# Kernel tuning notes

Hardware: AMD Instinct MI355X
Metric: run time of the kernel (lower is better)

The kernel has to match this reference:

```python
import jax, jax.numpy as jnp
import numpy as np

N, C, R = 8192, 512, 8
DK = C // R  # 64

def setup_inputs() -> dict:
    key = jax.random.key(0)
    k1, k2, kq, kk, kv = jax.random.split(key, 5)
    s = 0.05
    return {
        "im1": jax.random.normal(k1, (N, C), jnp.float32),
        "im2": jax.random.normal(k2, (N, C), jnp.float32),
        "Wq": jax.random.normal(kq, (C, DK), jnp.float32) * s,
        "Wk": jax.random.normal(kk, (C, DK), jnp.float32) * s,
        "Wv": jax.random.normal(kv, (C, C), jnp.float32) * s,
    }

def reference(im1, im2, Wq, Wk, Wv):
    # shared projections (weights stored as [in, out]; torch Linear is x @ W.T)
    im1_q = im1 @ Wq  # [N, DK]
    im1_k = im1 @ Wk  # [N, DK]
    im1_v = im1 @ Wv  # [N, C]
    im2_q = im2 @ Wq
    im2_k = im2 @ Wk
    im2_v = im2 @ Wv
    # cross attention (no scaling in original)
    im1_attn = jax.nn.softmax(im2_q @ im1_k.T, axis=-1)  # [N, N]
    im2_attn = jax.nn.softmax(im1_q @ im2_k.T, axis=-1)  # [N, N]
    im1_out = im1_attn @ im1_v + im1
    im2_out = im2_attn @ im2_v + im2
    return im1_out, im2_out
```

## Files before the change

### kernel.cpp

```cpp
#include <hip/hip_runtime.h>

#define NN 8192
#define CC 512
#define DKK 64

typedef float f32x4 __attribute__((ext_vector_type(4)));
typedef float f32x16 __attribute__((ext_vector_type(16)));
typedef _Float16 f16x8 __attribute__((ext_vector_type(8)));
typedef _Float16 f16x4 __attribute__((ext_vector_type(4)));

__device__ __forceinline__ f32x4 mfma16(f16x8 a, f16x8 b, f32x4 c) {
    return __builtin_amdgcn_mfma_f32_16x16x32_f16(a, b, c, 0, 0, 0);
}
__device__ __forceinline__ f32x16 mfma32(f16x8 a, f16x8 b, f32x16 c) {
    return __builtin_amdgcn_mfma_f32_32x32x16_f16(a, b, c, 0, 0, 0);
}
__device__ __forceinline__ f16x8 scl8(f16x8 v, float f) {
    _Float16 h = (_Float16)f;
    f16x8 r;
#pragma unroll
    for (int i = 0; i < 8; i++) r[i] = v[i] * h;
    return r;
}

__global__ void wtrans_all_kernel(const float* __restrict__ Wq, const float* __restrict__ Wk,
                                  const float* __restrict__ Wv,
                                  _Float16* __restrict__ Wqt, _Float16* __restrict__ Wkt,
                                  _Float16* __restrict__ Wvf) {
    int idx = blockIdx.x * 256 + threadIdx.x;
    if (idx < 32768) {
        int n = idx >> 9, k = idx & 511;
        Wqt[idx] = (_Float16)Wq[k * 64 + n];
    } else if (idx < 65536) {
        int j = idx - 32768;
        int n = j >> 9, k = j & 511;
        Wkt[j] = (_Float16)Wk[k * 64 + n];
    } else {
        int j = idx - 65536;
        int k16 = j & 15, c = (j >> 4) & 511, ks = j >> 13;
        Wvf[j] = (_Float16)Wv[(size_t)(16 * ks + k16) * 512 + c];
    }
}

__global__ __launch_bounds__(256) void proj_qk2_kernel(
    const float* __restrict__ im1, const float* __restrict__ im2,
    const _Float16* __restrict__ Wqt, const _Float16* __restrict__ Wkt,
    _Float16* __restrict__ Q1, _Float16* __restrict__ Kf1,
    _Float16* __restrict__ Q2, _Float16* __restrict__ Kf2)
{
    const float* X = blockIdx.y ? im2 : im1;
    _Float16* Q = blockIdx.y ? Q2 : Q1;
    _Float16* Kf = blockIdx.y ? Kf2 : Kf1;

    __shared__ __align__(16) _Float16 Wlds[128 * 512];

    const int tid = threadIdx.x;
    const int lane = tid & 63, wave = tid >> 6;
    const int n16 = lane & 15, quad = lane >> 4;

#pragma unroll
    for (int i = 0; i < 32; i++) {
        const int idx = tid + 256 * i;
        const int row = idx >> 6, ch = idx & 63;
        const _Float16* src = (row < 64) ? (Wqt + (size_t)row * 512 + ch * 8)
                                         : (Wkt + (size_t)(row - 64) * 512 + ch * 8);
        *(f16x8*)&Wlds[row * 512 + ((ch ^ (row & 7)) * 8)] = *(const f16x8*)src;
    }
    __syncthreads();

    const int arow = blockIdx.x * 64 + wave * 16 + n16;
    f32x4 acc[8];
#pragma unroll
    for (int i = 0; i < 8; i++) acc[i] = (f32x4){0.f, 0.f, 0.f, 0.f};

    const float* xbase = X + (size_t)arow * 512 + quad * 8;
    for (int kk = 0; kk < 16; kk++) {
        f32x4 xa = *(const f32x4*)(xbase + kk * 32);
        f32x4 xb = *(const f32x4*)(xbase + kk * 32 + 4);
        f16x8 afrag;
#pragma unroll
        for (int j = 0; j < 4; j++) { afrag[j] = (_Float16)xa[j]; afrag[4 + j] = (_Float16)xb[j]; }
#pragma unroll
        for (int t = 0; t < 8; t++) {
            const int row = t * 16 + n16;
            f16x8 bfr = *(const f16x8*)&Wlds[row * 512 + (((4 * kk + quad) ^ (row & 7)) * 8)];
            acc[t] = mfma16(afrag, bfr, acc[t]);
        }
    }
    const int rbase = blockIdx.x * 64 + wave * 16 + quad * 4;
#pragma unroll
    for (int t = 0; t < 4; t++)
#pragma unroll
        for (int r = 0; r < 4; r++) {
            Q[(size_t)(rbase + r) * 64 + t * 16 + n16] = (_Float16)acc[t][r];
            Kf[((size_t)(blockIdx.x * 4 + t) * 64 + (wave * 16 + quad * 4 + r)) * 16 + n16] =
                (_Float16)acc[4 + t][r];
        }
}

__global__ __launch_bounds__(256) void proj_vt_kernel(
    const float* __restrict__ im1, const float* __restrict__ im2,
    const _Float16* __restrict__ Wvf,
    _Float16* __restrict__ Vf1, _Float16* __restrict__ Vf2)
{
    const float* X = blockIdx.y ? im2 : im1;
    _Float16* Vf = blockIdx.y ? Vf2 : Vf1;
    const int n0 = blockIdx.x * 32;
    const int tid = threadIdx.x;
    const int lane = tid & 63, wave = tid >> 6;
    const int l31 = lane & 31, lhi = lane >> 5;

    __shared__ __align__(16) _Float16 Xlds[32 * 512];

#pragma unroll
    for (int i = 0; i < 8; i++) {
        const int n = tid >> 3;
        const int chunk = (tid & 7) + 8 * i;
        const float* xp = X + (size_t)(n0 + n) * CC + chunk * 8;
        f32x4 x0 = *(const f32x4*)xp;
        f32x4 x1 = *(const f32x4*)(xp + 4);
        f16x8 d;
#pragma unroll
        for (int j = 0; j < 4; j++) { d[j] = (_Float16)x0[j]; d[4 + j] = (_Float16)x1[j]; }
        *(f16x8*)&Xlds[n * 512 + ((chunk ^ (n & 7)) * 8)] = d;
    }
    __syncthreads();

    f32x16 acc[4];
#pragma unroll
    for (int t = 0; t < 4; t++)
#pragma unroll
        for (int r = 0; r < 16; r++) acc[t][r] = 0.f;

    for (int ks = 0; ks < 32; ks++) {
        f16x8 xb = *(const f16x8*)&Xlds[l31 * 512 + (((2 * ks + lhi) ^ (l31 & 7)) * 8)];
#pragma unroll
        for (int ct = 0; ct < 4; ct++) {
            const _Float16* wp = Wvf + ((size_t)ks * 512 + 128 * wave + 32 * ct + l31) * 16 + 8 * lhi;
            acc[ct] = mfma32(*(const f16x8*)wp, xb, acc[ct]);
        }
    }
    const int tile = n0 >> 6;
    const int ksbase = (n0 & 32) >> 4;
#pragma unroll
    for (int ct = 0; ct < 4; ct++)
#pragma unroll
        for (int r = 0; r < 16; r++) {
            const int c = 128 * wave + 32 * ct + (r & 3) + 8 * (r >> 2) + 4 * lhi;
            const int ks = ksbase + (l31 >> 4);
            Vf[((size_t)(tile * 4 + ks) * 512 + c) * 16 + (l31 & 15)] = (_Float16)acc[ct][r];
        }
}

__global__ __launch_bounds__(1024, 4) void flash7_kernel(
    const _Float16* __restrict__ Q1, const _Float16* __restrict__ Kf1,
    const _Float16* __restrict__ Q2, const _Float16* __restrict__ Kf2,
    const _Float16* __restrict__ Vf1, const _Float16* __restrict__ Vf2,
    const float* __restrict__ im1, const float* __restrict__ im2,
    float* __restrict__ out)
{
    const int bid = blockIdx.x;
    const int img = bid & 1;
    const int qbase = (bid >> 1) * 64;
    const _Float16* Q = img ? Q1 : Q2;
    const _Float16* Kf = img ? Kf2 : Kf1;
    const _Float16* Vf = img ? Vf2 : Vf1;
    const float* res = img ? im2 : im1;
    float* o = out + (size_t)img * NN * CC;

    __shared__ __align__(16) _Float16 P[2][4][8][64][8];
    __shared__ float mPart[2][4][2][64];
    __shared__ float mF[4][2][64], lF[4][2][64];

    const int tid = threadIdx.x;
    const int lane = tid & 63, w = tid >> 6;
    const int l31 = lane & 31, lhi = lane >> 5;
    const int g = w >> 2, a = (w >> 1) & 1, b = w & 1;

    f16x8 qf[4];
    {
        const _Float16* qp = Q + (size_t)(qbase + 32 * b + l31) * DKK + 8 * lhi;
#pragma unroll
        for (int k = 0; k < 4; k++) qf[k] = *(const f16x8*)(qp + 16 * k);
    }

    f32x16 acc[2];
#pragma unroll
    for (int t = 0; t < 2; t++)
#pragma unroll
        for (int r = 0; r < 16; r++) acc[t][r] = 0.f;

    float ma_run = -3e38f, l_run = 0.f;
    float mg_run[2] = {-3e38f, -3e38f};

    const _Float16* kb = Kf + ((size_t)(32 * a + l31)) * 16 + 8 * lhi;
    const _Float16* vb = Vf + ((size_t)(32 * w + l31)) * 16 + 8 * lhi;

    auto do_qk = [&](int s) {
        const int t = 4 * s + g;
        const int pbuf = s & 1;
        f32x16 sA;
#pragma unroll
        for (int r = 0; r < 16; r++) sA[r] = 0.f;
#pragma unroll
        for (int k = 0; k < 4; k++) {
            f16x8 kf = *(const f16x8*)(kb + (size_t)(t * 4 + k) * (64 * 16));
            sA = mfma32(kf, qf[k], sA);
        }
        float mr[8];
#pragma unroll
        for (int i = 0; i < 8; i++) mr[i] = fmaxf(sA[i], sA[i + 8]);
#pragma unroll
        for (int i = 0; i < 4; i++) mr[i] = fmaxf(mr[i], mr[i + 4]);
        float mx = fmaxf(fmaxf(mr[0], mr[1]), fmaxf(mr[2], mr[3]));
        mx = fmaxf(mx, __shfl_xor(mx, 32));
        const float manew = fmaxf(ma_run, mx);
        if (lane < 32) mPart[pbuf][g][a][32 * b + lane] = manew;
        float ls = 0.f;
#pragma unroll
        for (int r = 0; r < 16; r++) {
            float p = __expf(sA[r] - manew);
            ls += p;
            sA[r] = p;
        }
        ls += __shfl_xor(ls, 32);
        l_run = l_run * __expf(ma_run - manew) + ls;
        ma_run = manew;
#pragma unroll
        for (int gg = 0; gg < 4; gg++) {
            f16x4 p4;
#pragma unroll
            for (int u = 0; u < 4; u++) p4[u] = (_Float16)sA[gg * 4 + u];
            *(f16x4*)&P[pbuf][g][4 * a + gg][32 * b + l31][4 * lhi] = p4;
        }
    };

    do_qk(0);
    __syncthreads();

    for (int s = 0; s < 32; s++) {
        const int pbuf = s & 1;

        f16x8 va0[4];
#pragma unroll
        for (int tt = 0; tt < 4; tt++)
            va0[tt] = *(const f16x8*)(vb + ((size_t)((4 * s + tt) * 4) * 512) * 16);

        if (s < 31) do_qk(s + 1);

        float f[2][4][2];
        bool nos1 = true;
        float al[2];
#pragma unroll
        for (int qh = 0; qh < 2; qh++) {
            float mgn = mg_run[qh];
#pragma unroll
            for (int g2 = 0; g2 < 4; g2++)
#pragma unroll
                for (int a2 = 0; a2 < 2; a2++) {
                    f[qh][g2][a2] = mPart[pbuf][g2][a2][32 * qh + l31];
                    mgn = fmaxf(mgn, f[qh][g2][a2]);
                }
            al[qh] = __expf(mg_run[qh] - mgn);
            mg_run[qh] = mgn;
#pragma unroll
            for (int g2 = 0; g2 < 4; g2++)
#pragma unroll
                for (int a2 = 0; a2 < 2; a2++) {
                    f[qh][g2][a2] = __expf(f[qh][g2][a2] - mgn);
                    nos1 &= (f[qh][g2][a2] == 1.f);
                }
        }
        if (!__all((al[0] == 1.f) & (al[1] == 1.f))) {
#pragma unroll
            for (int qh = 0; qh < 2; qh++)
#pragma unroll
                for (int r = 0; r < 16; r++) acc[qh][r] *= al[qh];
        }
        const bool nos = __all(nos1);

#pragma unroll
        for (int tt = 0; tt < 4; tt++)
#pragma unroll
            for (int k = 0; k < 4; k++) {
                f16x8 pb0 = *(const f16x8*)&P[pbuf][tt][2 * k + lhi][l31][0];
                f16x8 pb1 = *(const f16x8*)&P[pbuf][tt][2 * k + lhi][32 + l31][0];
                if (!nos) {
                    pb0 = scl8(pb0, f[0][tt][k >> 1]);
                    pb1 = scl8(pb1, f[1][tt][k >> 1]);
                }
                f16x8 va = (k == 0) ? va0[tt]
                    : *(const f16x8*)(vb + ((size_t)((4 * s + tt) * 4 + k) * 512) * 16);
                acc[0] = mfma32(va, pb0, acc[0]);
                acc[1] = mfma32(va, pb1, acc[1]);
            }
        __syncthreads();
    }

    if (lane < 32) {
        mF[g][a][32 * b + lane] = ma_run;
        lF[g][a][32 * b + lane] = l_run;
    }
    __syncthreads();

    float fac[2];
#pragma unroll
    for (int qh = 0; qh < 2; qh++) {
        const int q = 32 * qh + l31;
        const float M = mg_run[qh];
        float den = 0.f;
#pragma unroll
        for (int g2 = 0; g2 < 4; g2++)
#pragma unroll
            for (int a2 = 0; a2 < 2; a2++)
                den += lF[g2][a2][q] * __expf(mF[g2][a2][q] - M);
        fac[qh] = 1.f / den;
    }

#pragma unroll
    for (int qh = 0; qh < 2; qh++)
#pragma unroll
        for (int rg = 0; rg < 4; rg++) {
            const int c = 32 * w + 8 * rg + 4 * lhi;
            const size_t off = (size_t)(qbase + 32 * qh + l31) * CC + c;
            f32x4 v;
#pragma unroll
            for (int u = 0; u < 4; u++) v[u] = acc[qh][4 * rg + u] * fac[qh];
            f32x4 r4 = *(const f32x4*)(res + off);
            *(f32x4*)(o + off) = v + r4;
        }
}

extern "C" void kernel_launch(void* const* d_in, const int* in_sizes, int n_in,
                              void* d_out, int out_size, void* d_ws, size_t ws_size,
                              hipStream_t stream) {
    const float* im1 = (const float*)d_in[0];
    const float* im2 = (const float*)d_in[1];
    const float* Wq  = (const float*)d_in[2];
    const float* Wk  = (const float*)d_in[3];
    const float* Wv  = (const float*)d_in[4];
    float* out = (float*)d_out;

    _Float16* w = (_Float16*)d_ws;
    _Float16* Wqt = w;
    _Float16* Wkt = Wqt + 64 * 512;
    _Float16* Wvf = Wkt + 64 * 512;
    _Float16* Q1  = Wvf + 512 * 512;
    _Float16* Kf1 = Q1 + NN * DKK;
    _Float16* Q2  = Kf1 + NN * DKK;
    _Float16* Kf2 = Q2 + NN * DKK;
    _Float16* Vf1 = Kf2 + NN * DKK;
    _Float16* Vf2 = Vf1 + (size_t)CC * NN;

    wtrans_all_kernel<<<1280, 256, 0, stream>>>(Wq, Wk, Wv, Wqt, Wkt, Wvf);
    proj_qk2_kernel<<<dim3(128, 2), 256, 0, stream>>>(im1, im2, Wqt, Wkt, Q1, Kf1, Q2, Kf2);
    proj_vt_kernel<<<dim3(256, 2), 256, 0, stream>>>(im1, im2, Wvf, Vf1, Vf2);
    flash7_kernel<<<256, 1024, 0, stream>>>(Q1, Kf1, Q2, Kf2, Vf1, Vf2, im1, im2, out);
}
```

Measured before the change: 363.1 us.

## Split flash attention output channels across blocks and use exp2 softmax

The attention kernel now launches 512 blocks of 512 threads instead of 256 blocks of 1024. Each block covers one half of the 512 value channels, and each wave computes both 32-key sub-tiles of its QK chunk. Q is pre-scaled by log2(e) in the projection so the softmax can use exp2 instead of exp. The skip-rescale branch for P is removed and the scale is applied unconditionally in half precision. The cost is that the QK and softmax work is duplicated across the two channel-half blocks, in exchange for more blocks to spread across the GPU and less exp overhead.

```diff
diff --git a/kernel.cpp b/kernel.cpp
--- a/kernel.cpp
+++ b/kernel.cpp
@@ -15,13 +15,13 @@
 __device__ __forceinline__ f32x16 mfma32(f16x8 a, f16x8 b, f32x16 c) {
     return __builtin_amdgcn_mfma_f32_32x32x16_f16(a, b, c, 0, 0, 0);
 }
-__device__ __forceinline__ f16x8 scl8(f16x8 v, float f) {
-    _Float16 h = (_Float16)f;
+__device__ __forceinline__ f16x8 sclh8(f16x8 v, _Float16 h) {
     f16x8 r;
 #pragma unroll
     for (int i = 0; i < 8; i++) r[i] = v[i] * h;
     return r;
 }
+__device__ __forceinline__ float exp2fast(float x) { return __builtin_exp2f(x); }
 
 __global__ void wtrans_all_kernel(const float* __restrict__ Wq, const float* __restrict__ Wk,
                                   const float* __restrict__ Wv,
@@ -92,7 +92,7 @@
     for (int t = 0; t < 4; t++)
 #pragma unroll
         for (int r = 0; r < 4; r++) {
-            Q[(size_t)(rbase + r) * 64 + t * 16 + n16] = (_Float16)acc[t][r];
+            Q[(size_t)(rbase + r) * 64 + t * 16 + n16] = (_Float16)(acc[t][r] * 1.44269504f);
             Kf[((size_t)(blockIdx.x * 4 + t) * 64 + (wave * 16 + quad * 4 + r)) * 16 + n16] =
                 (_Float16)acc[4 + t][r];
         }
@@ -152,7 +152,7 @@
         }
 }
 
-__global__ __launch_bounds__(1024, 4) void flash7_kernel(
+__global__ __launch_bounds__(512, 4) void flash15_kernel(
     const _Float16* __restrict__ Q1, const _Float16* __restrict__ Kf1,
     const _Float16* __restrict__ Q2, const _Float16* __restrict__ Kf2,
     const _Float16* __restrict__ Vf1, const _Float16* __restrict__ Vf2,
@@ -161,7 +161,8 @@
 {
     const int bid = blockIdx.x;
     const int img = bid & 1;
-    const int qbase = (bid >> 1) * 64;
+    const int chalf = (bid >> 1) & 1;
+    const int qbase = (bid >> 2) * 64;
     const _Float16* Q = img ? Q1 : Q2;
     const _Float16* Kf = img ? Kf2 : Kf1;
     const _Float16* Vf = img ? Vf2 : Vf1;
@@ -175,7 +176,7 @@
     const int tid = threadIdx.x;
     const int lane = tid & 63, w = tid >> 6;
     const int l31 = lane & 31, lhi = lane >> 5;
-    const int g = w >> 2, a = (w >> 1) & 1, b = w & 1;
+    const int g = w >> 1, b = w & 1;
 
     f16x8 qf[4];
     {
@@ -190,48 +191,51 @@
 #pragma unroll
         for (int r = 0; r < 16; r++) acc[t][r] = 0.f;
 
-    float ma_run = -3e38f, l_run = 0.f;
+    float ma_run[2] = {-3e38f, -3e38f}, l_run[2] = {0.f, 0.f};
     float mg_run[2] = {-3e38f, -3e38f};
 
-    const _Float16* kb = Kf + ((size_t)(32 * a + l31)) * 16 + 8 * lhi;
-    const _Float16* vb = Vf + ((size_t)(32 * w + l31)) * 16 + 8 * lhi;
+    const _Float16* kb = Kf + (size_t)l31 * 16 + 8 * lhi;
+    const _Float16* vb = Vf + (size_t)(256 * chalf + 32 * w + l31) * 16 + 8 * lhi;
 
     auto do_qk = [&](int s) {
         const int t = 4 * s + g;
         const int pbuf = s & 1;
-        f32x16 sA;
-#pragma unroll
-        for (int r = 0; r < 16; r++) sA[r] = 0.f;
-#pragma unroll
-        for (int k = 0; k < 4; k++) {
-            f16x8 kf = *(const f16x8*)(kb + (size_t)(t * 4 + k) * (64 * 16));
-            sA = mfma32(kf, qf[k], sA);
-        }
-        float mr[8];
-#pragma unroll
-        for (int i = 0; i < 8; i++) mr[i] = fmaxf(sA[i], sA[i + 8]);
-#pragma unroll
-        for (int i = 0; i < 4; i++) mr[i] = fmaxf(mr[i], mr[i + 4]);
-        float mx = fmaxf(fmaxf(mr[0], mr[1]), fmaxf(mr[2], mr[3]));
-        mx = fmaxf(mx, __shfl_xor(mx, 32));
-        const float manew = fmaxf(ma_run, mx);
-        if (lane < 32) mPart[pbuf][g][a][32 * b + lane] = manew;
-        float ls = 0.f;
-#pragma unroll
-        for (int r = 0; r < 16; r++) {
-            float p = __expf(sA[r] - manew);
-            ls += p;
-            sA[r] = p;
-        }
-        ls += __shfl_xor(ls, 32);
-        l_run = l_run * __expf(ma_run - manew) + ls;
-        ma_run = manew;
-#pragma unroll
-        for (int gg = 0; gg < 4; gg++) {
-            f16x4 p4;
-#pragma unroll
-            for (int u = 0; u < 4; u++) p4[u] = (_Float16)sA[gg * 4 + u];
-            *(f16x4*)&P[pbuf][g][4 * a + gg][32 * b + l31][4 * lhi] = p4;
+#pragma unroll
+        for (int a2 = 0; a2 < 2; a2++) {
+            f32x16 sA;
+#pragma unroll
+            for (int r = 0; r < 16; r++) sA[r] = 0.f;
+#pragma unroll
+            for (int k = 0; k < 4; k++) {
+                f16x8 kf = *(const f16x8*)(kb + (size_t)((t * 4 + k) * 64 + 32 * a2) * 16);
+                sA = mfma32(kf, qf[k], sA);
+            }
+            float mr[8];
+#pragma unroll
+            for (int i = 0; i < 8; i++) mr[i] = fmaxf(sA[i], sA[i + 8]);
+#pragma unroll
+            for (int i = 0; i < 4; i++) mr[i] = fmaxf(mr[i], mr[i + 4]);
+            float mx = fmaxf(fmaxf(mr[0], mr[1]), fmaxf(mr[2], mr[3]));
+            mx = fmaxf(mx, __shfl_xor(mx, 32));
+            const float manew = fmaxf(ma_run[a2], mx);
+            if (lane < 32) mPart[pbuf][g][a2][32 * b + lane] = manew;
+            float ls = 0.f;
+#pragma unroll
+            for (int r = 0; r < 16; r++) {
+                float p = exp2fast(sA[r] - manew);
+                ls += p;
+                sA[r] = p;
+            }
+            ls += __shfl_xor(ls, 32);
+            l_run[a2] = l_run[a2] * exp2fast(ma_run[a2] - manew) + ls;
+            ma_run[a2] = manew;
+#pragma unroll
+            for (int gg = 0; gg < 4; gg++) {
+                f16x4 p4;
+#pragma unroll
+                for (int u = 0; u < 4; u++) p4[u] = (_Float16)sA[gg * 4 + u];
+                *(f16x4*)&P[pbuf][g][4 * a2 + gg][32 * b + l31][4 * lhi] = p4;
+            }
         }
     };
 
@@ -244,12 +248,11 @@
         f16x8 va0[4];
 #pragma unroll
         for (int tt = 0; tt < 4; tt++)
-            va0[tt] = *(const f16x8*)(vb + ((size_t)((4 * s + tt) * 4) * 512) * 16);
+            va0[tt] = *(const f16x8*)(vb + (size_t)((4 * s + tt) * 4 * 512) * 16);
 
         if (s < 31) do_qk(s + 1);
 
         float f[2][4][2];
-        bool nos1 = true;
         float al[2];
 #pragma unroll
         for (int qh = 0; qh < 2; qh++) {
@@ -261,15 +264,13 @@
                     f[qh][g2][a2] = mPart[pbuf][g2][a2][32 * qh + l31];
                     mgn = fmaxf(mgn, f[qh][g2][a2]);
                 }
-            al[qh] = __expf(mg_run[qh] - mgn);
+            al[qh] = exp2fast(mg_run[qh] - mgn);
             mg_run[qh] = mgn;
 #pragma unroll
             for (int g2 = 0; g2 < 4; g2++)
 #pragma unroll
-                for (int a2 = 0; a2 < 2; a2++) {
-                    f[qh][g2][a2] = __expf(f[qh][g2][a2] - mgn);
-                    nos1 &= (f[qh][g2][a2] == 1.f);
-                }
+                for (int a2 = 0; a2 < 2; a2++)
+                    f[qh][g2][a2] = exp2fast(f[qh][g2][a2] - mgn);
         }
         if (!__all((al[0] == 1.f) & (al[1] == 1.f))) {
 #pragma unroll
@@ -277,7 +278,6 @@
 #pragma unroll
                 for (int r = 0; r < 16; r++) acc[qh][r] *= al[qh];
         }
-        const bool nos = __all(nos1);
 
 #pragma unroll
         for (int tt = 0; tt < 4; tt++)
@@ -285,12 +285,10 @@
             for (int k = 0; k < 4; k++) {
                 f16x8 pb0 = *(const f16x8*)&P[pbuf][tt][2 * k + lhi][l31][0];
                 f16x8 pb1 = *(const f16x8*)&P[pbuf][tt][2 * k + lhi][32 + l31][0];
-                if (!nos) {
-                    pb0 = scl8(pb0, f[0][tt][k >> 1]);
-                    pb1 = scl8(pb1, f[1][tt][k >> 1]);
-                }
+                pb0 = sclh8(pb0, (_Float16)f[0][tt][k >> 1]);
+                pb1 = sclh8(pb1, (_Float16)f[1][tt][k >> 1]);
                 f16x8 va = (k == 0) ? va0[tt]
-                    : *(const f16x8*)(vb + ((size_t)((4 * s + tt) * 4 + k) * 512) * 16);
+                    : *(const f16x8*)(vb + (size_t)(((4 * s + tt) * 4 + k) * 512) * 16);
                 acc[0] = mfma32(va, pb0, acc[0]);
                 acc[1] = mfma32(va, pb1, acc[1]);
             }
@@ -298,8 +296,11 @@
     }
 
     if (lane < 32) {
-        mF[g][a][32 * b + lane] = ma_run;
-        lF[g][a][32 * b + lane] = l_run;
+#pragma unroll
+        for (int a2 = 0; a2 < 2; a2++) {
+            mF[g][a2][32 * b + lane] = ma_run[a2];
+            lF[g][a2][32 * b + lane] = l_run[a2];
+        }
     }
     __syncthreads();
 
@@ -313,7 +314,7 @@
         for (int g2 = 0; g2 < 4; g2++)
 #pragma unroll
             for (int a2 = 0; a2 < 2; a2++)
-                den += lF[g2][a2][q] * __expf(mF[g2][a2][q] - M);
+                den += lF[g2][a2][q] * exp2fast(mF[g2][a2][q] - M);
         fac[qh] = 1.f / den;
     }
 
@@ -321,7 +322,7 @@
     for (int qh = 0; qh < 2; qh++)
 #pragma unroll
         for (int rg = 0; rg < 4; rg++) {
-            const int c = 32 * w + 8 * rg + 4 * lhi;
+            const int c = 256 * chalf + 32 * w + 8 * rg + 4 * lhi;
             const size_t off = (size_t)(qbase + 32 * qh + l31) * CC + c;
             f32x4 v;
 #pragma unroll
@@ -355,5 +356,5 @@
     wtrans_all_kernel<<<1280, 256, 0, stream>>>(Wq, Wk, Wv, Wqt, Wkt, Wvf);
     proj_qk2_kernel<<<dim3(128, 2), 256, 0, stream>>>(im1, im2, Wqt, Wkt, Q1, Kf1, Q2, Kf2);
     proj_vt_kernel<<<dim3(256, 2), 256, 0, stream>>>(im1, im2, Wvf, Vf1, Vf2);
-    flash7_kernel<<<256, 1024, 0, stream>>>(Q1, Kf1, Q2, Kf2, Vf1, Vf2, im1, im2, out);
-}
+    flash15_kernel<<<512, 512, 0, stream>>>(Q1, Kf1, Q2, Kf2, Vf1, Vf2, im1, im2, out);
+}
```

New measurement: 439.4 us. 1.21x slower.

## Stage V tiles through LDS and specialize waves for QK in flash attention

Applied to the files above, without the earlier changes.

The flash attention kernel now copies each 64-key V tile cooperatively into a double-buffered LDS buffer. The copy is issued one step ahead, and its LDS write happens after the PV MMAs. Only 4 of the 16 waves compute QK scores, with K prefetched into registers, and the loop takes 128 single-tile steps instead of 32 four-tile steps. Q is pre-scaled by log2(e) so exp2 replaces exp. The aim is to cut redundant global V reads and exp cost, at the price of more barriers, 64KB of LDS per block and idle waves during QK.

```diff
diff --git a/kernel.cpp b/kernel.cpp
--- a/kernel.cpp
+++ b/kernel.cpp
@@ -15,13 +15,13 @@
 __device__ __forceinline__ f32x16 mfma32(f16x8 a, f16x8 b, f32x16 c) {
     return __builtin_amdgcn_mfma_f32_32x32x16_f16(a, b, c, 0, 0, 0);
 }
-__device__ __forceinline__ f16x8 scl8(f16x8 v, float f) {
-    _Float16 h = (_Float16)f;
+__device__ __forceinline__ f16x8 sclh8(f16x8 v, _Float16 h) {
     f16x8 r;
 #pragma unroll
     for (int i = 0; i < 8; i++) r[i] = v[i] * h;
     return r;
 }
+__device__ __forceinline__ float exp2fast(float x) { return __builtin_exp2f(x); }
 
 __global__ void wtrans_all_kernel(const float* __restrict__ Wq, const float* __restrict__ Wk,
                                   const float* __restrict__ Wv,
@@ -92,7 +92,7 @@
     for (int t = 0; t < 4; t++)
 #pragma unroll
         for (int r = 0; r < 4; r++) {
-            Q[(size_t)(rbase + r) * 64 + t * 16 + n16] = (_Float16)acc[t][r];
+            Q[(size_t)(rbase + r) * 64 + t * 16 + n16] = (_Float16)(acc[t][r] * 1.44269504f);
             Kf[((size_t)(blockIdx.x * 4 + t) * 64 + (wave * 16 + quad * 4 + r)) * 16 + n16] =
                 (_Float16)acc[4 + t][r];
         }
@@ -152,7 +152,7 @@
         }
 }
 
-__global__ __launch_bounds__(1024, 4) void flash7_kernel(
+__global__ __launch_bounds__(1024, 4) void flash17_kernel(
     const _Float16* __restrict__ Q1, const _Float16* __restrict__ Kf1,
     const _Float16* __restrict__ Q2, const _Float16* __restrict__ Kf2,
     const _Float16* __restrict__ Vf1, const _Float16* __restrict__ Vf2,
@@ -168,44 +168,64 @@
     const float* res = img ? im2 : im1;
     float* o = out + (size_t)img * NN * CC;
 
-    __shared__ __align__(16) _Float16 P[2][4][8][64][8];
-    __shared__ float mPart[2][4][2][64];
-    __shared__ float mF[4][2][64], lF[4][2][64];
+    __shared__ __align__(16) _Float16 Vs[2][4 * 512 * 16];
+    __shared__ __align__(16) _Float16 P[2][8][64][8];
+    __shared__ float mPart[2][2][64];
+    __shared__ float mF[2][64], lF[2][64];
 
     const int tid = threadIdx.x;
     const int lane = tid & 63, w = tid >> 6;
     const int l31 = lane & 31, lhi = lane >> 5;
-    const int g = w >> 2, a = (w >> 1) & 1, b = w & 1;
-
-    f16x8 qf[4];
-    {
+    const bool isqk = (w < 4);
+    const int a = w & 1, b = (w >> 1) & 1;
+
+    f32x16 acc[2];
+#pragma unroll
+    for (int t = 0; t < 2; t++)
+#pragma unroll
+        for (int r = 0; r < 16; r++) acc[t][r] = 0.f;
+    float mg_run[2] = {-3e38f, -3e38f};
+
+    f16x8 qf[4], kreg[4];
+    float ma_run = -3e38f, l_run = 0.f;
+
+    const _Float16* kb = Kf + (size_t)(32 * a + l31) * 16 + 8 * lhi;
+
+    if (isqk) {
         const _Float16* qp = Q + (size_t)(qbase + 32 * b + l31) * DKK + 8 * lhi;
 #pragma unroll
         for (int k = 0; k < 4; k++) qf[k] = *(const f16x8*)(qp + 16 * k);
-    }
-
-    f32x16 acc[2];
-#pragma unroll
-    for (int t = 0; t < 2; t++)
-#pragma unroll
-        for (int r = 0; r < 16; r++) acc[t][r] = 0.f;
-
-    float ma_run = -3e38f, l_run = 0.f;
-    float mg_run[2] = {-3e38f, -3e38f};
-
-    const _Float16* kb = Kf + ((size_t)(32 * a + l31)) * 16 + 8 * lhi;
-    const _Float16* vb = Vf + ((size_t)(32 * w + l31)) * 16 + 8 * lhi;
-
-    auto do_qk = [&](int s) {
-        const int t = 4 * s + g;
-        const int pbuf = s & 1;
+#pragma unroll
+        for (int k = 0; k < 4; k++) kreg[k] = *(const f16x8*)(kb + (size_t)k * 1024);
+    }
+
+    f16x8 st0, st1, st2, st3;
+    auto stage_issue = [&](int t) {
+        const _Float16* src = Vf + (size_t)t * 32768 + w * 2048 + lane * 8;
+        st0 = *(const f16x8*)(src);
+        st1 = *(const f16x8*)(src + 512);
+        st2 = *(const f16x8*)(src + 1024);
+        st3 = *(const f16x8*)(src + 1536);
+    };
+    auto stage_write = [&](int t) {
+        _Float16* dst = &Vs[t & 1][0] + w * 2048 + lane * 8;
+        *(f16x8*)(dst) = st0;
+        *(f16x8*)(dst + 512) = st1;
+        *(f16x8*)(dst + 1024) = st2;
+        *(f16x8*)(dst + 1536) = st3;
+    };
+
+    auto do_qk = [&](int tt) {
+        const int pbuf = tt & 1;
         f32x16 sA;
 #pragma unroll
         for (int r = 0; r < 16; r++) sA[r] = 0.f;
 #pragma unroll
-        for (int k = 0; k < 4; k++) {
-            f16x8 kf = *(const f16x8*)(kb + (size_t)(t * 4 + k) * (64 * 16));
-            sA = mfma32(kf, qf[k], sA);
+        for (int k = 0; k < 4; k++) sA = mfma32(kreg[k], qf[k], sA);
+        if (tt + 1 < 128) {
+#pragma unroll
+            for (int k = 0; k < 4; k++)
+                kreg[k] = *(const f16x8*)(kb + (size_t)((tt + 1) * 4 + k) * 1024);
         }
         float mr[8];
 #pragma unroll
@@ -215,61 +235,51 @@
         float mx = fmaxf(fmaxf(mr[0], mr[1]), fmaxf(mr[2], mr[3]));
         mx = fmaxf(mx, __shfl_xor(mx, 32));
         const float manew = fmaxf(ma_run, mx);
-        if (lane < 32) mPart[pbuf][g][a][32 * b + lane] = manew;
+        if (lane < 32) mPart[pbuf][a][32 * b + lane] = manew;
         float ls = 0.f;
 #pragma unroll
         for (int r = 0; r < 16; r++) {
-            float p = __expf(sA[r] - manew);
+            float p = exp2fast(sA[r] - manew);
             ls += p;
             sA[r] = p;
         }
         ls += __shfl_xor(ls, 32);
-        l_run = l_run * __expf(ma_run - manew) + ls;
+        l_run = l_run * exp2fast(ma_run - manew) + ls;
         ma_run = manew;
 #pragma unroll
         for (int gg = 0; gg < 4; gg++) {
             f16x4 p4;
 #pragma unroll
             for (int u = 0; u < 4; u++) p4[u] = (_Float16)sA[gg * 4 + u];
-            *(f16x4*)&P[pbuf][g][4 * a + gg][32 * b + l31][4 * lhi] = p4;
+            *(f16x4*)&P[pbuf][4 * a + gg][32 * b + l31][4 * lhi] = p4;
         }
     };
 
-    do_qk(0);
+    stage_issue(0);
+    if (isqk) do_qk(0);
+    stage_write(0);
     __syncthreads();
 
-    for (int s = 0; s < 32; s++) {
+    for (int s = 0; s < 128; s++) {
         const int pbuf = s & 1;
-
-        f16x8 va0[4];
-#pragma unroll
-        for (int tt = 0; tt < 4; tt++)
-            va0[tt] = *(const f16x8*)(vb + ((size_t)((4 * s + tt) * 4) * 512) * 16);
-
-        if (s < 31) do_qk(s + 1);
-
-        float f[2][4][2];
-        bool nos1 = true;
-        float al[2];
+        if (s < 127) {
+            stage_issue(s + 1);
+            if (isqk) do_qk(s + 1);
+        }
+
+        float f[2][2], al[2];
 #pragma unroll
         for (int qh = 0; qh < 2; qh++) {
             float mgn = mg_run[qh];
 #pragma unroll
-            for (int g2 = 0; g2 < 4; g2++)
-#pragma unroll
-                for (int a2 = 0; a2 < 2; a2++) {
-                    f[qh][g2][a2] = mPart[pbuf][g2][a2][32 * qh + l31];
-                    mgn = fmaxf(mgn, f[qh][g2][a2]);
-                }
-            al[qh] = __expf(mg_run[qh] - mgn);
+            for (int a2 = 0; a2 < 2; a2++) {
+                f[qh][a2] = mPart[pbuf][a2][32 * qh + l31];
+                mgn = fmaxf(mgn, f[qh][a2]);
+            }
+            al[qh] = exp2fast(mg_run[qh] - mgn);
             mg_run[qh] = mgn;
 #pragma unroll
-            for (int g2 = 0; g2 < 4; g2++)
-#pragma unroll
-                for (int a2 = 0; a2 < 2; a2++) {
-                    f[qh][g2][a2] = __expf(f[qh][g2][a2] - mgn);
-                    nos1 &= (f[qh][g2][a2] == 1.f);
-                }
+            for (int a2 = 0; a2 < 2; a2++) f[qh][a2] = exp2fast(f[qh][a2] - mgn);
         }
         if (!__all((al[0] == 1.f) & (al[1] == 1.f))) {
 #pragma unroll
@@ -277,29 +287,26 @@
 #pragma unroll
                 for (int r = 0; r < 16; r++) acc[qh][r] *= al[qh];
         }
-        const bool nos = __all(nos1);
-
-#pragma unroll
-        for (int tt = 0; tt < 4; tt++)
-#pragma unroll
-            for (int k = 0; k < 4; k++) {
-                f16x8 pb0 = *(const f16x8*)&P[pbuf][tt][2 * k + lhi][l31][0];
-                f16x8 pb1 = *(const f16x8*)&P[pbuf][tt][2 * k + lhi][32 + l31][0];
-                if (!nos) {
-                    pb0 = scl8(pb0, f[0][tt][k >> 1]);
-                    pb1 = scl8(pb1, f[1][tt][k >> 1]);
-                }
-                f16x8 va = (k == 0) ? va0[tt]
-                    : *(const f16x8*)(vb + ((size_t)((4 * s + tt) * 4 + k) * 512) * 16);
-                acc[0] = mfma32(va, pb0, acc[0]);
-                acc[1] = mfma32(va, pb1, acc[1]);
-            }
+
+        const _Float16* vbufp = &Vs[pbuf][0];
+#pragma unroll
+        for (int ks = 0; ks < 4; ks++) {
+            f16x8 va = *(const f16x8*)(vbufp + ks * 8192 + (32 * w + l31) * 16 + 8 * lhi);
+            f16x8 pb0 = *(const f16x8*)&P[pbuf][2 * ks + lhi][l31][0];
+            f16x8 pb1 = *(const f16x8*)&P[pbuf][2 * ks + lhi][32 + l31][0];
+            pb0 = sclh8(pb0, (_Float16)f[0][ks >> 1]);
+            pb1 = sclh8(pb1, (_Float16)f[1][ks >> 1]);
+            acc[0] = mfma32(va, pb0, acc[0]);
+            acc[1] = mfma32(va, pb1, acc[1]);
+        }
+
+        if (s < 127) stage_write(s + 1);
         __syncthreads();
     }
 
-    if (lane < 32) {
-        mF[g][a][32 * b + lane] = ma_run;
-        lF[g][a][32 * b + lane] = l_run;
+    if (isqk && lane < 32) {
+        mF[a][32 * b + lane] = ma_run;
+        lF[a][32 * b + lane] = l_run;
     }
     __syncthreads();
 
@@ -310,10 +317,8 @@
         const float M = mg_run[qh];
         float den = 0.f;
 #pragma unroll
-        for (int g2 = 0; g2 < 4; g2++)
-#pragma unroll
-            for (int a2 = 0; a2 < 2; a2++)
-                den += lF[g2][a2][q] * __expf(mF[g2][a2][q] - M);
+        for (int a2 = 0; a2 < 2; a2++)
+            den += lF[a2][q] * exp2fast(mF[a2][q] - M);
         fac[qh] = 1.f / den;
     }
 
@@ -355,5 +360,5 @@
     wtrans_all_kernel<<<1280, 256, 0, stream>>>(Wq, Wk, Wv, Wqt, Wkt, Wvf);
     proj_qk2_kernel<<<dim3(128, 2), 256, 0, stream>>>(im1, im2, Wqt, Wkt, Q1, Kf1, Q2, Kf2);
     proj_vt_kernel<<<dim3(256, 2), 256, 0, stream>>>(im1, im2, Wvf, Vf1, Vf2);
-    flash7_kernel<<<256, 1024, 0, stream>>>(Q1, Kf1, Q2, Kf2, Vf1, Vf2, im1, im2, out);
-}
+    flash17_kernel<<<256, 1024, 0, stream>>>(Q1, Kf1, Q2, Kf2, Vf1, Vf2, im1, im2, out);
+}
```

Result: slower. 388.7 us (+7.0%).
